# Kernel tuning notes

Measured on AMD Instinct MI355X. Metric: run time of the kernel, lower is better.

The kernel has to match this reference:

```python
import jax, jax.numpy as jnp
import numpy as np

D_MODEL = 1024
HEADS = 16
DEPTH = D_MODEL // HEADS
B, S = 4, 4096
EPS_K = 1e-6  # kernel feature epsilon
EPS_LN = 1e-6


def setup_inputs() -> dict:
    key = jax.random.key(0)
    ks = jax.random.split(key, 8)
    lecun = 1.0 / np.sqrt(D_MODEL)  # LecunNormal stddev
    glorot = np.sqrt(2.0 / (D_MODEL + D_MODEL))  # keras Dense default
    return {
        "q": jax.random.normal(ks[0], (B, S, D_MODEL), jnp.float32),
        "k": jax.random.normal(ks[1], (B, S, D_MODEL), jnp.float32),
        "v": jax.random.normal(ks[2], (B, S, D_MODEL), jnp.float32),
        "mask": jnp.ones((B, S), jnp.float32),
        "wq": jax.random.normal(ks[3], (D_MODEL, D_MODEL), jnp.float32) * lecun,
        "wk": jax.random.normal(ks[4], (D_MODEL, D_MODEL), jnp.float32) * lecun,
        "wv": jax.random.normal(ks[5], (D_MODEL, D_MODEL), jnp.float32) * lecun,
        "ln_gamma": jnp.ones((D_MODEL,), jnp.float32),
        "ln_beta": jnp.zeros((D_MODEL,), jnp.float32),
        "dense_w": jax.random.normal(ks[6], (D_MODEL, D_MODEL), jnp.float32) * glorot,
        "dense_b": jnp.zeros((D_MODEL,), jnp.float32),
    }


def _layernorm(x, g, b):
    m = jnp.mean(x, axis=-1, keepdims=True)
    var = jnp.var(x, axis=-1, keepdims=True)
    return (x - m) * jax.lax.rsqrt(var + EPS_LN) * g + b


def _split_heads(x):
    bsz, sl, _ = x.shape
    return x.reshape(bsz, sl, HEADS, DEPTH).transpose(0, 2, 1, 3)  # [B,H,S,depth]


def reference(q, k, v, mask, wq, wk, wv, ln_gamma, ln_beta, dense_w, dense_b):
    bsz = q.shape[0]
    em = mask[:, None, :, None]  # [B,1,S,1] broadcast over heads/depth
    qh = _split_heads(_layernorm(q @ wq, ln_gamma, ln_beta))
    kh = _split_heads(_layernorm(k @ wk, ln_gamma, ln_beta))
    vh = _split_heads(_layernorm(v @ wv, ln_gamma, ln_beta))
    q_prime = jax.nn.relu(qh) + EPS_K
    k_prime = (jax.nn.relu(kh) + EPS_K) * em
    vh = vh * em
    kv = jnp.einsum('bhnd,bhne->bhde', k_prime, vh)  # [B,H,depth,depth]
    z = 1.0 / (jnp.einsum('bhnd,bhd->bhn', q_prime, k_prime.sum(axis=-2)) + EPS_K)
    att = jnp.einsum('bhnd,bhde,bhn->bhne', q_prime, kv, z)  # [B,H,S,depth]
    # Faithful to original: reshape WITHOUT transposing heads back.
    att = att.reshape(bsz, -1, D_MODEL)  # [B,S,d_model]
    out = att @ dense_w + dense_b
    return _layernorm(out, ln_gamma, ln_beta)
```

## Files before the change

kernel.cpp:

```cpp
#include <hip/hip_runtime.h>
#include <hip/hip_bf16.h>
#include <stdint.h>

#define D_MODEL 1024
#define S_LEN   4096
#define BATCH   4
#define HEADS   16
#define DEPTH   64
#define ROWS    (BATCH*S_LEN)
#define EPS_K_F 1e-6f
#define EPS_LN_F 1e-6f

typedef __attribute__((ext_vector_type(8))) short short8;
typedef __attribute__((ext_vector_type(4))) float f32x4;

__device__ __forceinline__ unsigned short f2bf(float f) {
  union { float f; unsigned u; } x; x.f = f;
  unsigned r = x.u + 0x7FFF + ((x.u >> 16) & 1);
  return (unsigned short)(r >> 16);
}
__device__ __forceinline__ float bf2f(unsigned short b) {
  union { unsigned u; float f; } x; x.u = ((unsigned)b) << 16;
  return x.f;
}
__device__ __forceinline__ void gload16(const void* g, void* l) {
  __builtin_amdgcn_global_load_lds(
      (const __attribute__((address_space(1))) void*)g,
      (__attribute__((address_space(3))) void*)l, 16, 0, 0);
}

__global__ __launch_bounds__(256) void wtrans_k(
    const float* __restrict__ W, unsigned short* __restrict__ Wt,
    const float* __restrict__ qsrc, unsigned short* __restrict__ qdst,
    int slice) {
  __shared__ float tile[32][33];
  int n0 = blockIdx.x * 32, k0 = blockIdx.y * 32;
  int tx = threadIdx.x & 31, ty = threadIdx.x >> 5;
  #pragma unroll
  for (int i = 0; i < 32; i += 8)
    tile[ty + i][tx] = W[(size_t)(k0 + ty + i) * D_MODEL + n0 + tx];
  if (qsrc) {
    int bid = blockIdx.y * 32 + blockIdx.x;
    size_t base = (size_t)slice * 4194304 + (size_t)bid * 4096 +
                  (size_t)threadIdx.x * 8;
    #pragma unroll
    for (int it = 0; it < 2; ++it) {
      size_t off = base + (size_t)it * 2048;
      float4 a = *(const float4*)(qsrc + off);
      float4 b = *(const float4*)(qsrc + off + 4);
      uint4 pk;
      pk.x = (unsigned)f2bf(a.x) | ((unsigned)f2bf(a.y) << 16);
      pk.y = (unsigned)f2bf(a.z) | ((unsigned)f2bf(a.w) << 16);
      pk.z = (unsigned)f2bf(b.x) | ((unsigned)f2bf(b.y) << 16);
      pk.w = (unsigned)f2bf(b.z) | ((unsigned)f2bf(b.w) << 16);
      *(uint4*)(qdst + off) = pk;
    }
  }
  __syncthreads();
  #pragma unroll
  for (int i = 0; i < 32; i += 8)
    Wt[(size_t)(n0 + ty + i) * D_MODEL + k0 + tx] = f2bf(tile[tx][ty + i]);
}


#define GEMM_EPILOGUE(HASBIAS)                                               \
  if (HASBIAS) {                                                             \
    float bv[4];                                                             \
    _Pragma("unroll")                                                        \
    for (int n = 0; n < 4; ++n)                                              \
      bv[n] = bias[(int)n0 + wcn * 64 + n * 16 + l15];                       \
    _Pragma("unroll")                                                        \
    for (int m = 0; m < 8; ++m)                                              \
      _Pragma("unroll")                                                      \
      for (int n = 0; n < 4; ++n)                                            \
        _Pragma("unroll")                                                    \
        for (int j = 0; j < 4; ++j)                                          \
          acc[m][n][j] += bv[n];                                             \
  }                                                                          \
  int seg = (int)(n0 >> 6) + wcn;                                            \
  _Pragma("unroll")                                                          \
  for (int m = 0; m < 8; ++m) {                                              \
    float s[4], s2[4];                                                       \
    _Pragma("unroll")                                                        \
    for (int j = 0; j < 4; ++j) {                                            \
      float a = 0.f, b = 0.f;                                                \
      _Pragma("unroll")                                                      \
      for (int n = 0; n < 4; ++n) { float x = acc[m][n][j]; a += x; b += x*x; } \
      s[j] = a; s2[j] = b;                                                   \
    }                                                                        \
    _Pragma("unroll")                                                        \
    for (int off = 1; off < 16; off <<= 1) {                                 \
      _Pragma("unroll")                                                      \
      for (int j = 0; j < 4; ++j) {                                          \
        s[j]  += __shfl_xor(s[j],  off);                                     \
        s2[j] += __shfl_xor(s2[j], off);                                     \
      }                                                                      \
    }                                                                        \
    if (l15 == 0) {                                                          \
      _Pragma("unroll")                                                      \
      for (int j = 0; j < 4; ++j) {                                          \
        int rg = (int)m0 + wr * 128 + m * 16 + lhi * 4 + j;                  \
        psum[rg * 16 + seg] = s[j];                                          \
        psq [rg * 16 + seg] = s2[j];                                         \
      }                                                                      \
    }                                                                        \
  }                                                                          \
  _Pragma("unroll")                                                          \
  for (int m = 0; m < 8; ++m)                                                \
    _Pragma("unroll")                                                        \
    for (int j = 0; j < 4; ++j) {                                            \
      size_t row = m0 + wr * 128 + m * 16 + lhi * 4 + j;                     \
      _Pragma("unroll")                                                      \
      for (int n = 0; n < 4; ++n) {                                          \
        int col = (int)n0 + wcn * 64 + n * 16 + l15;                         \
        Cb[row * N + col] = f2bf(acc[m][n][j]);                              \
      }                                                                      \
    }

#define STAGE_HALF(kof_, slot_, h_) do {                                     \
    _Pragma("unroll")                                                        \
    for (int j = 0; j < 2; ++j) {                                            \
      int idx = j * 512 + t; int r_ = idx >> 2; int cs_ = idx & 3;           \
      int c_ = cs_ ^ ((r_ >> 1) & 3);                                        \
      gload16(A + (m0 + r_) * (size_t)K + (kof_) + (h_) * 32 + c_ * 8,       \
              &Al[slot_][(h_) * 8192 + idx * 8]);                            \
    }                                                                        \
    _Pragma("unroll")                                                        \
    for (int j = 0; j < 2; ++j) {                                            \
      int idx = j * 512 + t; int r_ = idx >> 2; int cs_ = idx & 3;           \
      int c_ = cs_ ^ ((r_ >> 1) & 3);                                        \
      gload16(Bt + (n0 + r_) * (size_t)K + (kof_) + (h_) * 32 + c_ * 8,      \
              &Bl[slot_][(h_) * 8192 + idx * 8]);                            \
    }                                                                        \
  } while (0)

#define PH_READ_B(kk_)                                                       \
    _Pragma("unroll")                                                        \
    for (int n = 0; n < 4; ++n) {                                            \
      int rb_ = wcn * 64 + n * 16 + l15;                                     \
      bfr[n] = *(const short8*)&Bl[slot][(kk_) * 8192 + rb_ * 32 + cswz];    \
    }
#define PH_READ_A(kk_, mh_)                                                  \
    _Pragma("unroll")                                                        \
    for (int m = 0; m < 4; ++m) {                                            \
      int ra_ = wr * 128 + ((mh_) * 4 + m) * 16 + l15;                       \
      af[m] = *(const short8*)&Al[slot][(kk_) * 8192 + ra_ * 32 + cswz];     \
    }
#define PH_MFMA(mh_)                                                         \
    __builtin_amdgcn_s_setprio(1);                                           \
    _Pragma("unroll")                                                        \
    for (int m = 0; m < 4; ++m)                                              \
      _Pragma("unroll")                                                      \
      for (int n = 0; n < 4; ++n)                                            \
        acc[(mh_) * 4 + m][n] = __builtin_amdgcn_mfma_f32_16x16x32_bf16(     \
            af[m], bfr[n], acc[(mh_) * 4 + m][n], 0, 0, 0);                  \
    __builtin_amdgcn_s_setprio(0);
#define LGKM0                                                                \
    asm volatile("s_waitcnt lgkmcnt(0)" ::: "memory");                       \
    __builtin_amdgcn_sched_barrier(0);

#define SIDE_PACK_STORE(chunk_) do {                                         \
    uint4 pk_;                                                               \
    pk_.x = (unsigned)f2bf(sreg0.x) | ((unsigned)f2bf(sreg0.y) << 16);       \
    pk_.y = (unsigned)f2bf(sreg0.z) | ((unsigned)f2bf(sreg0.w) << 16);       \
    pk_.z = (unsigned)f2bf(sreg1.x) | ((unsigned)f2bf(sreg1.y) << 16);       \
    pk_.w = (unsigned)f2bf(sreg1.z) | ((unsigned)f2bf(sreg1.w) << 16);       \
    *(uint4*)(side_dst + sbase + (size_t)(chunk_) * 4096) = pk_;             \
  } while (0)
#define SIDE_LOAD(chunk_) do {                                               \
    const float* sp_ = side_src + sbase + (size_t)(chunk_) * 4096;           \
    sreg0 = *(const float4*)sp_; sreg1 = *(const float4*)(sp_ + 4);          \
  } while (0)

#define TAIL_TILE(slot_) do {                                                \
    const int slot = (slot_);                                                \
    short8 af[4], bfr[4];                                                    \
    PH_READ_B(0) PH_READ_A(0, 0) LGKM0 PH_MFMA(0)                            \
    PH_READ_A(0, 1) LGKM0 PH_MFMA(1)                                         \
    PH_READ_B(1) PH_READ_A(1, 0) LGKM0 PH_MFMA(0)                            \
    PH_READ_A(1, 1) LGKM0 PH_MFMA(1)                                         \
  } while (0)

template <bool SIDECAR>
__global__ __launch_bounds__(512) void gemm_bt_k(
    const unsigned short* __restrict__ A,
    const unsigned short* __restrict__ Bt,
    unsigned short* __restrict__ Cb,
    float* __restrict__ psum, float* __restrict__ psq,
    const float* __restrict__ bias,
    const float* __restrict__ side_src,
    unsigned short* __restrict__ side_dst,
    int M, int N, int K) {
  __shared__ unsigned short Al[2][16384];
  __shared__ unsigned short Bl[2][16384];
  int t = threadIdx.x;
  int lane = t & 63, wid = t >> 6;
  int wr = wid >> 2, wcn = wid & 3;
  int l15 = lane & 15, lhi = lane >> 4;
  const int cswz = (lhi ^ ((l15 >> 1) & 3)) << 3;
  int p = blockIdx.x;
  int cb = (p >> 3) & 3;
  int rb = (p & 7) | ((p >> 5) << 3);
  size_t m0 = (size_t)rb * 256, n0 = (size_t)cb * 256;
  f32x4 acc[8][4] = {};

  const int KT = K >> 6;

  float4 sreg0 = {}, sreg1 = {};
  size_t sbase = (size_t)p * 65536 + (size_t)t * 8;

  if (SIDECAR) SIDE_LOAD(0);
  STAGE_HALF(0, 0, 0);  STAGE_HALF(0, 0, 1);
  STAGE_HALF(64, 1, 0); STAGE_HALF(64, 1, 1);
  asm volatile("s_waitcnt vmcnt(8)" ::: "memory");
  __builtin_amdgcn_s_barrier();
  __builtin_amdgcn_sched_barrier(0);

  for (int kt = 0; kt < KT - 2; ++kt) {
    const int slot = kt & 1;
    short8 af[4], bfr[4];
    PH_READ_B(0)
    PH_READ_A(0, 0)
    LGKM0
    PH_MFMA(0)
    PH_READ_A(0, 1)
    LGKM0
    __builtin_amdgcn_s_barrier();
    __builtin_amdgcn_sched_barrier(0);
    STAGE_HALF((kt + 2) << 6, slot, 0);
    __builtin_amdgcn_sched_barrier(0);
    PH_MFMA(1)
    PH_READ_B(1)
    PH_READ_A(1, 0)
    LGKM0
    PH_MFMA(0)
    PH_READ_A(1, 1)
    LGKM0
    __builtin_amdgcn_s_barrier();
    __builtin_amdgcn_sched_barrier(0);
    STAGE_HALF((kt + 2) << 6, slot, 1);
    __builtin_amdgcn_sched_barrier(0);
    PH_MFMA(1)
    if (SIDECAR) {
      SIDE_PACK_STORE(kt);
      SIDE_LOAD(kt + 1);
      __builtin_amdgcn_sched_barrier(0);
      asm volatile("s_waitcnt vmcnt(11)" ::: "memory");
    } else {
      asm volatile("s_waitcnt vmcnt(8)" ::: "memory");
    }
    __builtin_amdgcn_s_barrier();
    __builtin_amdgcn_sched_barrier(0);
  }

  TAIL_TILE((KT - 2) & 1);
  if (SIDECAR) {
    SIDE_PACK_STORE(KT - 2);
    SIDE_LOAD(KT - 1);
    __builtin_amdgcn_sched_barrier(0);
    asm volatile("s_waitcnt vmcnt(3)" ::: "memory");
  } else {
    asm volatile("s_waitcnt vmcnt(0)" ::: "memory");
  }
  __builtin_amdgcn_s_barrier();
  __builtin_amdgcn_sched_barrier(0);

  TAIL_TILE((KT - 1) & 1);
  if (SIDECAR) SIDE_PACK_STORE(KT - 1);

  GEMM_EPILOGUE(bias != nullptr)
}

__global__ __launch_bounds__(256) void ln_act_k(
    const unsigned short* __restrict__ Cb,
    const float* __restrict__ psum, const float* __restrict__ psq,
    const float* __restrict__ gamma, const float* __restrict__ beta,
    const float* __restrict__ mask,
    unsigned short* __restrict__ out, int mode) {
  int row = blockIdx.x;
  int t = threadIdx.x;
  float s = 0.f, s2 = 0.f;
  #pragma unroll
  for (int i = 0; i < 16; ++i) { s += psum[row * 16 + i]; s2 += psq[row * 16 + i]; }
  float mean = s * (1.f / D_MODEL);
  float var = s2 * (1.f / D_MODEL) - mean * mean;
  float rstd = rsqrtf(var + EPS_LN_F);
  float mk = (mode > 0) ? mask[row] : 1.f;
  ushort4 cv = ((const ushort4*)(Cb + (size_t)row * D_MODEL))[t];
  float4 gv = ((const float4*)gamma)[t];
  float4 bv = ((const float4*)beta)[t];
  float av[4] = {bf2f(cv.x), bf2f(cv.y), bf2f(cv.z), bf2f(cv.w)};
  float g4[4] = {gv.x, gv.y, gv.z, gv.w};
  float b4[4] = {bv.x, bv.y, bv.z, bv.w};
  unsigned short ov[4];
  #pragma unroll
  for (int j = 0; j < 4; ++j) {
    float ln = (av[j] - mean) * rstd * g4[j] + b4[j];
    if (mode == 0)      ln = fmaxf(ln, 0.f) + EPS_K_F;
    else if (mode == 1) ln = (fmaxf(ln, 0.f) + EPS_K_F) * mk;
    else                ln = ln * mk;
    ov[j] = f2bf(ln);
  }
  ushort4 o; o.x = ov[0]; o.y = ov[1]; o.z = ov[2]; o.w = ov[3];
  ((ushort4*)(out + (size_t)row * D_MODEL))[t] = o;
}

__global__ __launch_bounds__(256) void ln_final_k(
    const unsigned short* __restrict__ Cb,
    const float* __restrict__ psum, const float* __restrict__ psq,
    const float* __restrict__ gamma, const float* __restrict__ beta,
    float* __restrict__ out) {
  int row = blockIdx.x;
  int t = threadIdx.x;
  float s = 0.f, s2 = 0.f;
  #pragma unroll
  for (int i = 0; i < 16; ++i) { s += psum[row * 16 + i]; s2 += psq[row * 16 + i]; }
  float mean = s * (1.f / D_MODEL);
  float var = s2 * (1.f / D_MODEL) - mean * mean;
  float rstd = rsqrtf(var + EPS_LN_F);
  ushort4 cv = ((const ushort4*)(Cb + (size_t)row * D_MODEL))[t];
  float4 gv = ((const float4*)gamma)[t];
  float4 bv = ((const float4*)beta)[t];
  float4 w;
  w.x = (bf2f(cv.x) - mean) * rstd * gv.x + bv.x;
  w.y = (bf2f(cv.y) - mean) * rstd * gv.y + bv.y;
  w.z = (bf2f(cv.z) - mean) * rstd * gv.z + bv.z;
  w.w = (bf2f(cv.w) - mean) * rstd * gv.w + bv.w;
  ((float4*)(out + (size_t)row * D_MODEL))[t] = w;
}

__global__ __launch_bounds__(256) void kv_mfma_k(
    const unsigned short* __restrict__ Kp, const unsigned short* __restrict__ Vp,
    float* __restrict__ part, float* __restrict__ kspart) {
  __shared__ unsigned short Kl[4096];
  __shared__ unsigned short Vl[4096];
  int bh = blockIdx.y, chunk = blockIdx.x;
  int b_ = bh >> 4, h = bh & 15;
  int t = threadIdx.x, lane = t & 63, w = t >> 6;
  int l15 = lane & 15, g = lane >> 4;

  int sn = t >> 2, sd16 = t & 3;
  int sc = sd16 ^ ((sn >> 3) & 3);
  size_t goff = (size_t)sn * D_MODEL + h * DEPTH + sd16 * 16;
  int ldst = sn * 64 + sc * 16;

  short8 ones;
  #pragma unroll
  for (int i = 0; i < 8; ++i) ones[i] = (short)0x3F80;

  f32x4 acc[4] = {};
  f32x4 ks = {};

  int baseA = ((w ^ g) << 4) + l15;
  int baseB0 = ((0 ^ g) << 4) + l15;
  int baseB1 = ((1 ^ g) << 4) + l15;
  int baseB2 = ((2 ^ g) << 4) + l15;
  int baseB3 = ((3 ^ g) << 4) + l15;

  size_t rowbase = ((size_t)b_ * S_LEN + (size_t)chunk * 512) * D_MODEL;
  for (int tile = 0; tile < 8; ++tile) {
    const unsigned short* kg = Kp + rowbase + (size_t)tile * 64 * D_MODEL + goff;
    const unsigned short* vg = Vp + rowbase + (size_t)tile * 64 * D_MODEL + goff;
    uint4 ra = *(const uint4*)kg;
    uint4 rb = *(const uint4*)(kg + 8);
    uint4 rc = *(const uint4*)vg;
    uint4 rd = *(const uint4*)(vg + 8);
    __syncthreads();
    *(uint4*)&Kl[ldst]     = ra;
    *(uint4*)&Kl[ldst + 8] = rb;
    *(uint4*)&Vl[ldst]     = rc;
    *(uint4*)&Vl[ldst + 8] = rd;
    __syncthreads();
    #pragma unroll
    for (int kk = 0; kk < 2; ++kk) {
      int nb = (kk * 32 + g * 8) * 64;
      short8 af, bf0, bf1, bf2, bf3;
      #pragma unroll
      for (int i = 0; i < 8; ++i) {
        int rowoff = nb + i * 64;
        af[i]  = (short)Kl[rowoff + baseA];
        bf0[i] = (short)Vl[rowoff + baseB0];
        bf1[i] = (short)Vl[rowoff + baseB1];
        bf2[i] = (short)Vl[rowoff + baseB2];
        bf3[i] = (short)Vl[rowoff + baseB3];
      }
      acc[0] = __builtin_amdgcn_mfma_f32_16x16x32_bf16(af, bf0, acc[0], 0, 0, 0);
      acc[1] = __builtin_amdgcn_mfma_f32_16x16x32_bf16(af, bf1, acc[1], 0, 0, 0);
      acc[2] = __builtin_amdgcn_mfma_f32_16x16x32_bf16(af, bf2, acc[2], 0, 0, 0);
      acc[3] = __builtin_amdgcn_mfma_f32_16x16x32_bf16(af, bf3, acc[3], 0, 0, 0);
      ks     = __builtin_amdgcn_mfma_f32_16x16x32_bf16(af, ones, ks, 0, 0, 0);
    }
  }
  float* pp = part + ((size_t)bh * 8 + chunk) * 4096;
  #pragma unroll
  for (int nf = 0; nf < 4; ++nf)
    #pragma unroll
    for (int r = 0; r < 4; ++r)
      pp[(16 * w + 4 * g + r) * 64 + 16 * nf + l15] = acc[nf][r];
  if (l15 == 0) {
    #pragma unroll
    for (int r = 0; r < 4; ++r)
      kspart[((size_t)bh * 8 + chunk) * 64 + 16 * w + 4 * g + r] = ks[r];
  }
}

__global__ __launch_bounds__(256) void kv_reduce_k(
    const float* __restrict__ part, const float* __restrict__ kspart,
    unsigned short* __restrict__ KVT, float* __restrict__ ksum) {
  int bh = blockIdx.x, t = threadIdx.x;
  for (int idx = t; idx < 4096; idx += 256) {
    int d = idx >> 6, e = idx & 63;
    float s = 0.f;
    #pragma unroll
    for (int c = 0; c < 8; ++c)
      s += part[((size_t)bh * 8 + c) * 4096 + d * 64 + e];
    KVT[(size_t)bh * 4096 + e * 64 + d] = f2bf(s);
  }
  if (t < 64) {
    float s = 0.f;
    #pragma unroll
    for (int c = 0; c < 8; ++c) s += kspart[((size_t)bh * 8 + c) * 64 + t];
    ksum[bh * 64 + t] = s;
  }
}

__global__ __launch_bounds__(256) void att_k(
    const unsigned short* __restrict__ Qp, const unsigned short* __restrict__ KVT,
    const float* __restrict__ ksum, unsigned short* __restrict__ att) {
  __shared__ unsigned short Ql[128 * 64];
  __shared__ unsigned short Kl[64 * 64];
  __shared__ float ksl[64];
  __shared__ float zl[128];
  int bh = blockIdx.y;
  int b = bh >> 4, h = bh & 15;
  int r0 = blockIdx.x * 128;
  int t = threadIdx.x, lane = t & 63, wid = t >> 6;
  int l15 = lane & 15, lhi = lane >> 4;
  #pragma unroll
  for (int i = 0; i < 4; ++i) {
    int cid = i * 256 + t;
    int r = cid >> 3, c8 = cid & 7;
    gload16(Qp + ((size_t)(b * S_LEN + r0 + r)) * D_MODEL + h * DEPTH + c8 * 8,
            &Ql[cid * 8]);
  }
  #pragma unroll
  for (int i = 0; i < 2; ++i) {
    int cid = i * 256 + t;
    gload16(KVT + (size_t)bh * 4096 + cid * 8, &Kl[cid * 8]);
  }
  if (t < 64) ksl[t] = ksum[bh * 64 + t];
  asm volatile("s_waitcnt vmcnt(0)" ::: "memory");
  __syncthreads();
  {
    int r = t >> 1, half = t & 1;
    float s = 0.f;
    #pragma unroll
    for (int j = 0; j < 32; ++j)
      s += bf2f(Ql[r * 64 + half * 32 + j]) * ksl[half * 32 + j];
    s += __shfl_xor(s, 1);
    if (half == 0) zl[r] = 1.f / (s + EPS_K_F);
  }
  __syncthreads();
  f32x4 acc[2][4] = {};
  #pragma unroll
  for (int kk = 0; kk < 2; ++kk) {
    short8 af[2], bfr[4];
    #pragma unroll
    for (int m = 0; m < 2; ++m)
      af[m] = *(const short8*)&Ql[(wid * 32 + m * 16 + l15) * 64 + kk * 32 + lhi * 8];
    #pragma unroll
    for (int n = 0; n < 4; ++n)
      bfr[n] = *(const short8*)&Kl[(n * 16 + l15) * 64 + kk * 32 + lhi * 8];
    #pragma unroll
    for (int m = 0; m < 2; ++m)
      #pragma unroll
      for (int n = 0; n < 4; ++n)
        acc[m][n] = __builtin_amdgcn_mfma_f32_16x16x32_bf16(af[m], bfr[n], acc[m][n], 0, 0, 0);
  }
  #pragma unroll
  for (int m = 0; m < 2; ++m)
    #pragma unroll
    for (int j = 0; j < 4; ++j) {
      int rl = wid * 32 + m * 16 + lhi * 4 + j;
      int n = r0 + rl;
      float z = zl[rl];
      #pragma unroll
      for (int nf = 0; nf < 4; ++nf) {
        int ee = nf * 16 + l15;
        size_t orow = (size_t)b * S_LEN + h * 256 + (n >> 4);
        int ocol = (n & 15) * 64 + ee;
        att[orow * D_MODEL + ocol] = f2bf(acc[m][nf][j] * z);
      }
    }
}

extern "C" void kernel_launch(void* const* d_in, const int* in_sizes, int n_in,
                              void* d_out, int out_size, void* d_ws, size_t ws_size,
                              hipStream_t stream) {
  (void)in_sizes; (void)n_in; (void)out_size; (void)ws_size;
  const float* q     = (const float*)d_in[0];
  const float* k     = (const float*)d_in[1];
  const float* v     = (const float*)d_in[2];
  const float* mask  = (const float*)d_in[3];
  const float* wq    = (const float*)d_in[4];
  const float* wk    = (const float*)d_in[5];
  const float* wv    = (const float*)d_in[6];
  const float* gamma = (const float*)d_in[7];
  const float* beta  = (const float*)d_in[8];
  const float* dw    = (const float*)d_in[9];
  const float* db    = (const float*)d_in[10];
  float* out = (float*)d_out;

  char* ws = (char*)d_ws;
  unsigned short* Xq  = (unsigned short*)(ws);
  unsigned short* Xk  = (unsigned short*)(ws + 33554432);
  unsigned short* Xv  = (unsigned short*)(ws + 67108864);
  unsigned short* Qp  = Xq;
  unsigned short* Kp  = Xk;
  unsigned short* Vp  = Xv;
  unsigned short* Cd  = Xq;
  unsigned short* WqT = (unsigned short*)(ws + 100663296);
  unsigned short* WkT = WqT + 1048576;
  unsigned short* WvT = WkT + 1048576;
  unsigned short* WdT = WvT + 1048576;
  float* part   = (float*)(ws + 109051904);
  float* kspart = (float*)(ws + 117440512);
  unsigned short* KVT = (unsigned short*)(ws + 117964800);
  float* ksum = (float*)(ws + 118489088);
  float* psum = (float*)(ws + 119537664);
  float* psq  = (float*)(ws + 120586240);
  unsigned short* Cqkv = (unsigned short*)d_out;

  dim3 b256(256);
  dim3 b512(512);
  dim3 wtg(32, 32);
  dim3 gemmg(256);
  dim3 lng(ROWS);

  wtrans_k<<<wtg, b256, 0, stream>>>(wq, WqT, q, Xq, 0);
  wtrans_k<<<wtg, b256, 0, stream>>>(wk, WkT, q, Xq, 1);
  wtrans_k<<<wtg, b256, 0, stream>>>(wv, WvT, q, Xq, 2);
  wtrans_k<<<wtg, b256, 0, stream>>>(dw, WdT, q, Xq, 3);

  gemm_bt_k<true><<<gemmg, b512, 0, stream>>>(Xq, WqT, Cqkv, psum, psq, nullptr,
                                              k, Xk, ROWS, D_MODEL, D_MODEL);
  ln_act_k<<<lng, b256, 0, stream>>>(Cqkv, psum, psq, gamma, beta, nullptr, Qp, 0);

  gemm_bt_k<true><<<gemmg, b512, 0, stream>>>(Xk, WkT, Cqkv, psum, psq, nullptr,
                                              v, Xv, ROWS, D_MODEL, D_MODEL);
  ln_act_k<<<lng, b256, 0, stream>>>(Cqkv, psum, psq, gamma, beta, mask, Kp, 1);

  gemm_bt_k<false><<<gemmg, b512, 0, stream>>>(Xv, WvT, Cqkv, psum, psq, nullptr,
                                               nullptr, nullptr, ROWS, D_MODEL, D_MODEL);
  ln_act_k<<<lng, b256, 0, stream>>>(Cqkv, psum, psq, gamma, beta, mask, Vp, 2);

  kv_mfma_k<<<dim3(8, 64), b256, 0, stream>>>(Kp, Vp, part, kspart);
  kv_reduce_k<<<dim3(64), b256, 0, stream>>>(part, kspart, KVT, ksum);
  att_k<<<dim3(32, 64), b256, 0, stream>>>(Qp, KVT, ksum, Cqkv);

  gemm_bt_k<false><<<gemmg, b512, 0, stream>>>(Cqkv, WdT, Cd, psum, psq, db,
                                               nullptr, nullptr, ROWS, D_MODEL, D_MODEL);
  ln_final_k<<<lng, b256, 0, stream>>>(Cd, psum, psq, gamma, beta, out);
}
```

Before: 335.9 us.

## Fuse K/V layernorm, ReLU and mask into the KV reduction kernel

The K and V projection GEMMs now write raw outputs and partial statistics to separate buffers. A tiny kernel turns these into per-row mean and rstd. kv_mfma_k then applies layernorm, the feature map and the mask while staging tiles into LDS. This removes two full read/write passes over the K and V activations, at the cost of extra ALU work and per-row loads inside the KV accumulation kernel.

```diff
diff --git a/kernel.cpp b/kernel.cpp
--- a/kernel.cpp
+++ b/kernel.cpp
@@ -271,12 +271,31 @@
   GEMM_EPILOGUE(bias != nullptr)
 }
 
+__global__ __launch_bounds__(256) void ln_stats_k(
+    const float* __restrict__ psumK, const float* __restrict__ psqK,
+    const float* __restrict__ psumV, const float* __restrict__ psqV,
+    float* __restrict__ meanK, float* __restrict__ rstdK,
+    float* __restrict__ meanV, float* __restrict__ rstdV) {
+  int row = blockIdx.x * 256 + threadIdx.x;
+  float sK = 0.f, s2K = 0.f, sV = 0.f, s2V = 0.f;
+  #pragma unroll
+  for (int i = 0; i < 16; ++i) {
+    sK += psumK[row * 16 + i]; s2K += psqK[row * 16 + i];
+    sV += psumV[row * 16 + i]; s2V += psqV[row * 16 + i];
+  }
+  float mK = sK * (1.f / D_MODEL);
+  float mV = sV * (1.f / D_MODEL);
+  meanK[row] = mK;
+  rstdK[row] = rsqrtf(s2K * (1.f / D_MODEL) - mK * mK + EPS_LN_F);
+  meanV[row] = mV;
+  rstdV[row] = rsqrtf(s2V * (1.f / D_MODEL) - mV * mV + EPS_LN_F);
+}
+
 __global__ __launch_bounds__(256) void ln_act_k(
     const unsigned short* __restrict__ Cb,
     const float* __restrict__ psum, const float* __restrict__ psq,
     const float* __restrict__ gamma, const float* __restrict__ beta,
-    const float* __restrict__ mask,
-    unsigned short* __restrict__ out, int mode) {
+    unsigned short* __restrict__ out) {
   int row = blockIdx.x;
   int t = threadIdx.x;
   float s = 0.f, s2 = 0.f;
@@ -285,7 +304,6 @@
   float mean = s * (1.f / D_MODEL);
   float var = s2 * (1.f / D_MODEL) - mean * mean;
   float rstd = rsqrtf(var + EPS_LN_F);
-  float mk = (mode > 0) ? mask[row] : 1.f;
   ushort4 cv = ((const ushort4*)(Cb + (size_t)row * D_MODEL))[t];
   float4 gv = ((const float4*)gamma)[t];
   float4 bv = ((const float4*)beta)[t];
@@ -296,10 +314,7 @@
   #pragma unroll
   for (int j = 0; j < 4; ++j) {
     float ln = (av[j] - mean) * rstd * g4[j] + b4[j];
-    if (mode == 0)      ln = fmaxf(ln, 0.f) + EPS_K_F;
-    else if (mode == 1) ln = (fmaxf(ln, 0.f) + EPS_K_F) * mk;
-    else                ln = ln * mk;
-    ov[j] = f2bf(ln);
+    ov[j] = f2bf(fmaxf(ln, 0.f) + EPS_K_F);
   }
   ushort4 o; o.x = ov[0]; o.y = ov[1]; o.z = ov[2]; o.w = ov[3];
   ((ushort4*)(out + (size_t)row * D_MODEL))[t] = o;
@@ -330,7 +345,11 @@
 }
 
 __global__ __launch_bounds__(256) void kv_mfma_k(
-    const unsigned short* __restrict__ Kp, const unsigned short* __restrict__ Vp,
+    const unsigned short* __restrict__ Ck, const unsigned short* __restrict__ Cv,
+    const float* __restrict__ meanK, const float* __restrict__ rstdK,
+    const float* __restrict__ meanV, const float* __restrict__ rstdV,
+    const float* __restrict__ mask,
+    const float* __restrict__ gamma, const float* __restrict__ beta,
     float* __restrict__ part, float* __restrict__ kspart) {
   __shared__ unsigned short Kl[4096];
   __shared__ unsigned short Vl[4096];
@@ -344,6 +363,18 @@
   size_t goff = (size_t)sn * D_MODEL + h * DEPTH + sd16 * 16;
   int ldst = sn * 64 + sc * 16;
 
+  float g16[16], b16[16];
+  {
+    int cbase = h * DEPTH + sd16 * 16;
+    #pragma unroll
+    for (int i = 0; i < 4; ++i) {
+      float4 gv = *(const float4*)(gamma + cbase + i * 4);
+      float4 bv = *(const float4*)(beta + cbase + i * 4);
+      g16[i*4+0] = gv.x; g16[i*4+1] = gv.y; g16[i*4+2] = gv.z; g16[i*4+3] = gv.w;
+      b16[i*4+0] = bv.x; b16[i*4+1] = bv.y; b16[i*4+2] = bv.z; b16[i*4+3] = bv.w;
+    }
+  }
+
   short8 ones;
   #pragma unroll
   for (int i = 0; i < 8; ++i) ones[i] = (short)0x3F80;
@@ -357,19 +388,34 @@
   int baseB2 = ((2 ^ g) << 4) + l15;
   int baseB3 = ((3 ^ g) << 4) + l15;
 
-  size_t rowbase = ((size_t)b_ * S_LEN + (size_t)chunk * 512) * D_MODEL;
+  int rowbase_r = b_ * S_LEN + chunk * 512;
+  size_t rowbase = (size_t)rowbase_r * D_MODEL;
   for (int tile = 0; tile < 8; ++tile) {
-    const unsigned short* kg = Kp + rowbase + (size_t)tile * 64 * D_MODEL + goff;
-    const unsigned short* vg = Vp + rowbase + (size_t)tile * 64 * D_MODEL + goff;
+    const unsigned short* kg = Ck + rowbase + (size_t)tile * 64 * D_MODEL + goff;
+    const unsigned short* vg = Cv + rowbase + (size_t)tile * 64 * D_MODEL + goff;
     uint4 ra = *(const uint4*)kg;
     uint4 rb = *(const uint4*)(kg + 8);
     uint4 rc = *(const uint4*)vg;
     uint4 rd = *(const uint4*)(vg + 8);
+    int grow = rowbase_r + tile * 64 + sn;
+    float mk  = mask[grow];
+    float mKv = meanK[grow], rKv = rstdK[grow];
+    float mVv = meanV[grow], rVv = rstdV[grow];
+    union { uint4 u[2]; unsigned short s[16]; } kin, vin, kout, vout;
+    kin.u[0] = ra; kin.u[1] = rb;
+    vin.u[0] = rc; vin.u[1] = rd;
+    #pragma unroll
+    for (int j = 0; j < 16; ++j) {
+      float lnk = (bf2f(kin.s[j]) - mKv) * rKv * g16[j] + b16[j];
+      kout.s[j] = f2bf((fmaxf(lnk, 0.f) + EPS_K_F) * mk);
+      float lnv = (bf2f(vin.s[j]) - mVv) * rVv * g16[j] + b16[j];
+      vout.s[j] = f2bf(lnv * mk);
+    }
     __syncthreads();
-    *(uint4*)&Kl[ldst]     = ra;
-    *(uint4*)&Kl[ldst + 8] = rb;
-    *(uint4*)&Vl[ldst]     = rc;
-    *(uint4*)&Vl[ldst + 8] = rd;
+    *(uint4*)&Kl[ldst]     = kout.u[0];
+    *(uint4*)&Kl[ldst + 8] = kout.u[1];
+    *(uint4*)&Vl[ldst]     = vout.u[0];
+    *(uint4*)&Vl[ldst + 8] = vout.u[1];
     __syncthreads();
     #pragma unroll
     for (int kk = 0; kk < 2; ++kk) {
@@ -516,8 +562,6 @@
   unsigned short* Xk  = (unsigned short*)(ws + 33554432);
   unsigned short* Xv  = (unsigned short*)(ws + 67108864);
   unsigned short* Qp  = Xq;
-  unsigned short* Kp  = Xk;
-  unsigned short* Vp  = Xv;
   unsigned short* Cd  = Xq;
   unsigned short* WqT = (unsigned short*)(ws + 100663296);
   unsigned short* WkT = WqT + 1048576;
@@ -527,9 +571,20 @@
   float* kspart = (float*)(ws + 117440512);
   unsigned short* KVT = (unsigned short*)(ws + 117964800);
   float* ksum = (float*)(ws + 118489088);
-  float* psum = (float*)(ws + 119537664);
-  float* psq  = (float*)(ws + 120586240);
-  unsigned short* Cqkv = (unsigned short*)d_out;
+  float* psum  = (float*)(ws + 119537664);
+  float* psq   = (float*)(ws + 120586240);
+  float* psumK = (float*)(ws + 121634816);
+  float* psqK  = (float*)(ws + 122683392);
+  float* psumV = (float*)(ws + 123731968);
+  float* psqV  = (float*)(ws + 124780544);
+  float* meanK = (float*)(ws + 125829120);
+  float* rstdK = (float*)(ws + 125894656);
+  float* meanV = (float*)(ws + 125960192);
+  float* rstdV = (float*)(ws + 126025728);
+  unsigned short* Cq = (unsigned short*)d_out;
+  unsigned short* Ck = (unsigned short*)d_out;
+  unsigned short* Cv = (unsigned short*)((char*)d_out + 33554432);
+  unsigned short* Catt = (unsigned short*)d_out;
 
   dim3 b256(256);
   dim3 b512(512);
@@ -542,23 +597,24 @@
   wtrans_k<<<wtg, b256, 0, stream>>>(wv, WvT, q, Xq, 2);
   wtrans_k<<<wtg, b256, 0, stream>>>(dw, WdT, q, Xq, 3);
 
-  gemm_bt_k<true><<<gemmg, b512, 0, stream>>>(Xq, WqT, Cqkv, psum, psq, nullptr,
+  gemm_bt_k<true><<<gemmg, b512, 0, stream>>>(Xq, WqT, Cq, psum, psq, nullptr,
                                               k, Xk, ROWS, D_MODEL, D_MODEL);
-  ln_act_k<<<lng, b256, 0, stream>>>(Cqkv, psum, psq, gamma, beta, nullptr, Qp, 0);
-
-  gemm_bt_k<true><<<gemmg, b512, 0, stream>>>(Xk, WkT, Cqkv, psum, psq, nullptr,
+  ln_act_k<<<lng, b256, 0, stream>>>(Cq, psum, psq, gamma, beta, Qp);
+
+  gemm_bt_k<true><<<gemmg, b512, 0, stream>>>(Xk, WkT, Ck, psumK, psqK, nullptr,
                                               v, Xv, ROWS, D_MODEL, D_MODEL);
-  ln_act_k<<<lng, b256, 0, stream>>>(Cqkv, psum, psq, gamma, beta, mask, Kp, 1);
-
-  gemm_bt_k<false><<<gemmg, b512, 0, stream>>>(Xv, WvT, Cqkv, psum, psq, nullptr,
+  gemm_bt_k<false><<<gemmg, b512, 0, stream>>>(Xv, WvT, Cv, psumV, psqV, nullptr,
                                                nullptr, nullptr, ROWS, D_MODEL, D_MODEL);
-  ln_act_k<<<lng, b256, 0, stream>>>(Cqkv, psum, psq, gamma, beta, mask, Vp, 2);
-
-  kv_mfma_k<<<dim3(8, 64), b256, 0, stream>>>(Kp, Vp, part, kspart);
+
+  ln_stats_k<<<dim3(64), b256, 0, stream>>>(psumK, psqK, psumV, psqV,
+                                            meanK, rstdK, meanV, rstdV);
+
+  kv_mfma_k<<<dim3(8, 64), b256, 0, stream>>>(Ck, Cv, meanK, rstdK, meanV, rstdV,
+                                              mask, gamma, beta, part, kspart);
   kv_reduce_k<<<dim3(64), b256, 0, stream>>>(part, kspart, KVT, ksum);
-  att_k<<<dim3(32, 64), b256, 0, stream>>>(Qp, KVT, ksum, Cqkv);
-
-  gemm_bt_k<false><<<gemmg, b512, 0, stream>>>(Cqkv, WdT, Cd, psum, psq, db,
+  att_k<<<dim3(32, 64), b256, 0, stream>>>(Qp, KVT, ksum, Catt);
+
+  gemm_bt_k<false><<<gemmg, b512, 0, stream>>>(Catt, WdT, Cd, psum, psq, db,
                                                nullptr, nullptr, ROWS, D_MODEL, D_MODEL);
   ln_final_k<<<lng, b256, 0, stream>>>(Cd, psum, psq, gamma, beta, out);
 }
```

Measured after the change: 310.9 us. 7.4% less time.
